# Kernel tuning notes

Hardware: AMD Instinct MI355X
Metric: run time of the kernel (lower is better)

Reference implementation:

```python
import jax, jax.numpy as jnp
import numpy as np

N_NODES = 50000
N_EDGES = 800000
N_FEAT = 128
D_HID = 128
N_CLASS = 40


def gcn_conv(x, W, b, src, dst, n_nodes):
    """PyG GCNConv: h = D^{-1/2} (A + I) D^{-1/2} (x @ W) + b.
    src/dst are int arrays [E]; self-loops handled analytically."""
    h = x @ W  # [N, D]
    ones = jnp.ones(src.shape[0], dtype=h.dtype)
    # degree after adding self-loops: 1 + in-degree (edge weights are 1)
    deg = 1.0 + jax.ops.segment_sum(ones, dst, num_segments=n_nodes)
    dinv = jax.lax.rsqrt(deg)  # [N]
    # messages along edges src -> dst with symmetric normalization
    msg = h[src] * (dinv[src] * dinv[dst])[:, None]  # [E, D]
    agg = jax.ops.segment_sum(msg, dst, num_segments=n_nodes)  # [N, D]
    # self-loop contribution: dinv[i]^2 * h[i]
    agg = agg + h * (dinv * dinv)[:, None]
    return agg + b


def setup_inputs() -> dict:
    key = jax.random.key(0)
    ks = jax.random.split(key, 5)
    x = jax.random.normal(ks[0], (N_NODES, N_FEAT), dtype=jnp.float32)
    edge_index = jax.random.randint(ks[1], (2, N_EDGES), 0, N_NODES, dtype=jnp.int64)
    s_in = 1.0 / np.sqrt(N_FEAT)
    s_h = 1.0 / np.sqrt(D_HID)
    W_in = jax.random.normal(ks[2], (N_FEAT, D_HID), dtype=jnp.float32) * s_in
    W1 = jax.random.normal(ks[3], (D_HID, D_HID), dtype=jnp.float32) * s_h
    W_out = jax.random.normal(ks[4], (D_HID, N_CLASS), dtype=jnp.float32) * s_h
    return {
        "x": x,
        "edge_index": edge_index,
        "W_in": W_in,
        "b_in": jnp.zeros((D_HID,), jnp.float32),
        "W1": W1,
        "b1": jnp.zeros((D_HID,), jnp.float32),
        "W_out": W_out,
        "b_out": jnp.zeros((N_CLASS,), jnp.float32),
    }


def reference(x, edge_index, W_in, b_in, W1, b1, W_out, b_out):
    src, dst = edge_index[0], edge_index[1]
    n = x.shape[0]
    # input GCNConv (no activation on input_fc, matching the torch forward)
    h = gcn_conv(x, W_in, b_in, src, dst, n)
    # hidden layer: dropout is identity at eval; relu after conv; normalize=False
    h = jax.nn.relu(gcn_conv(h, W1, b1, src, dst, n))
    out = h @ W_out + b_out
    return jax.nn.log_softmax(out, axis=1)
```

## Files before the change

kernel.cpp:

```cpp
#include <hip/hip_runtime.h>
#include <math.h>


#define THREADS 256

typedef __attribute__((ext_vector_type(8))) short short8v;
typedef __attribute__((ext_vector_type(4))) float float4v;

__device__ __forceinline__ float b2f(unsigned int lo16) {
    return __uint_as_float(lo16 << 16);
}
__device__ __forceinline__ unsigned short f2b(float f) {
    unsigned int u = __float_as_uint(f);
    u += 0x7FFFu + ((u >> 16) & 1u);
    return (unsigned short)(u >> 16);
}

__global__ __launch_bounds__(256) void f_init(const float* __restrict__ x,
                                              const int* __restrict__ idx,
                                              const float* __restrict__ W0,
                                              const float* __restrict__ W1f,
                                              int* __restrict__ flag,
                                              int* __restrict__ cnt,
                                              uint4* __restrict__ wpk0,
                                              uint4* __restrict__ wpk1,
                                              unsigned short* __restrict__ Xb,
                                              int N) {
    int tid = threadIdx.x, bid = blockIdx.x, nb = gridDim.x;
    if (bid == 0 && tid < 64) {
        unsigned long long b = __ballot(idx[2 * tid + 1] == 0);
        if (tid == 0) *flag = (b == 0xFFFFFFFFFFFFFFFFull) ? 1 : 0;
    }
    for (int i = bid * 256 + tid; i < N; i += nb * 256) cnt[i] = 0;
    if (bid < 2) {
        const float* W = bid ? W1f : W0;
        uint4* wpk = bid ? wpk1 : wpk0;
#pragma unroll
        for (int it = 0; it < 8; ++it) {
            int s = it * 256 + tid;
            int ct = s >> 8, kb = (s >> 6) & 3, l = s & 63;
            int col = ct * 16 + (l & 15);
            int k0 = kb * 32 + ((l >> 4) << 3);
            uint4 u;
            u.x = (unsigned int)f2b(W[(k0 + 0) * 128 + col]) | ((unsigned int)f2b(W[(k0 + 1) * 128 + col]) << 16);
            u.y = (unsigned int)f2b(W[(k0 + 2) * 128 + col]) | ((unsigned int)f2b(W[(k0 + 3) * 128 + col]) << 16);
            u.z = (unsigned int)f2b(W[(k0 + 4) * 128 + col]) | ((unsigned int)f2b(W[(k0 + 5) * 128 + col]) << 16);
            u.w = (unsigned int)f2b(W[(k0 + 6) * 128 + col]) | ((unsigned int)f2b(W[(k0 + 7) * 128 + col]) << 16);
            wpk[s] = u;
        }
    }
    int total = N * 32;
    const float4* x4 = (const float4*)x;
    ushort4* xb4 = (ushort4*)Xb;
    for (int i = bid * 256 + tid; i < total; i += nb * 256) {
        float4 v = x4[i];
        ushort4 o;
        o.x = f2b(v.x); o.y = f2b(v.y); o.z = f2b(v.z); o.w = f2b(v.w);
        xb4[i] = o;
    }
}

__device__ __forceinline__ void gemm_body(const unsigned short* __restrict__ Ab,
                                          const uint4* __restrict__ wpk,
                                          unsigned short* __restrict__ outb,
                                          unsigned short* ol, int base, int N) {
    int tid = threadIdx.x;
    int w = tid >> 6, l = tid & 63;
    int lr = l & 15, lq = l >> 4;
    int arow0 = base + w * 16 + lr;
    int arow1 = base + 64 + w * 16 + lr;
    int ar0 = (arow0 < N) ? arow0 : (N - 1);
    int ar1 = (arow1 < N) ? arow1 : (N - 1);

    float4v acc[2][8];
#pragma unroll
    for (int t = 0; t < 2; ++t)
#pragma unroll
        for (int ct = 0; ct < 8; ++ct) acc[t][ct] = (float4v){0.f, 0.f, 0.f, 0.f};

#pragma unroll
    for (int kb = 0; kb < 4; ++kb) {
        uint4 v0 = *(const uint4*)(Ab + (size_t)ar0 * 128 + kb * 32 + lq * 8);
        uint4 v1 = *(const uint4*)(Ab + (size_t)ar1 * 128 + kb * 32 + lq * 8);
        union { uint4 u; short8v s; } c0, c1; c0.u = v0; c1.u = v1;
        short8v af0 = c0.s, af1 = c1.s;
#pragma unroll
        for (int ct = 0; ct < 8; ++ct) {
            uint4 bv = wpk[(ct * 4 + kb) * 64 + l];
            union { uint4 u; short8v s; } cv; cv.u = bv; short8v bf = cv.s;
            acc[0][ct] = __builtin_amdgcn_mfma_f32_16x16x32_bf16(af0, bf, acc[0][ct], 0, 0, 0);
            acc[1][ct] = __builtin_amdgcn_mfma_f32_16x16x32_bf16(af1, bf, acc[1][ct], 0, 0, 0);
        }
    }
#pragma unroll
    for (int t = 0; t < 2; ++t)
#pragma unroll
        for (int ct = 0; ct < 8; ++ct)
#pragma unroll
            for (int r = 0; r < 4; ++r)
                ol[(t * 64 + w * 16 + lq * 4 + r) * 128 + ct * 16 + lr] = f2b(acc[t][ct][r]);
    __syncthreads();
#pragma unroll
    for (int it = 0; it < 8; ++it) {
        int o = it * 4096 + tid * 16;
        int rr = o >> 8, cb = o & 255;
        int gr = base + rr;
        if (gr < N) {
            uint4 v = *(const uint4*)((const char*)ol + o);
            *(uint4*)((char*)outb + (size_t)gr * 256 + cb) = v;
        }
    }
}

__global__ __launch_bounds__(256) void f_g1fp(const unsigned short* __restrict__ Xb,
                                              const uint4* __restrict__ wpk1,
                                              unsigned short* __restrict__ B0,
                                              const int* __restrict__ idx,
                                              const int* __restrict__ flag,
                                              int* __restrict__ cnt,
                                              unsigned int* __restrict__ rec,
                                              int N, int E, int nbg) {
    __shared__ unsigned short ol[128 * 128];
    if ((int)blockIdx.x < nbg) {
        gemm_body(Xb, wpk1, B0, ol, blockIdx.x * 128, N);
        return;
    }
    int e = (blockIdx.x - nbg) * 256 + threadIdx.x;
    if (e >= E) return;
    int f = *flag;
    int src, dst;
    if (f) { src = idx[2 * e]; dst = idx[2 * (E + e)]; }
    else   { src = idx[e];     dst = idx[E + e]; }
    unsigned int pos = (unsigned int)atomicAdd(&cnt[dst], 1);
    rec[e] = ((unsigned int)src << 16) | (pos & 0xFFFFu);
}

__global__ __launch_bounds__(256) void gemm_mfma(const unsigned short* __restrict__ Ab,
                                                 const uint4* __restrict__ wpk,
                                                 unsigned short* __restrict__ outb,
                                                 int N) {
    __shared__ unsigned short ol[128 * 128];
    gemm_body(Ab, wpk, outb, ol, blockIdx.x * 128, N);
}

__global__ __launch_bounds__(256) void scanA(const int* __restrict__ cnt,
                                             int* __restrict__ bsum, int N) {
    __shared__ int wt[4];
    int tid = threadIdx.x, lane = tid & 63, w = tid >> 6;
    int i = blockIdx.x * 256 + tid;
    int v = (i < N) ? cnt[i] : 0;
    int s = v;
#pragma unroll
    for (int off = 1; off < 64; off <<= 1) {
        int t = __shfl_up(s, off);
        if (lane >= off) s += t;
    }
    if (lane == 63) wt[w] = s;
    __syncthreads();
    if (tid == 0) bsum[blockIdx.x] = wt[0] + wt[1] + wt[2] + wt[3];
}

__global__ __launch_bounds__(256) void scanB(int* __restrict__ bsum,
                                             int* __restrict__ boff,
                                             int* __restrict__ rowstart,
                                             int nb, int N) {
    __shared__ int wt[4];
    __shared__ int wo[5];
    int tid = threadIdx.x, lane = tid & 63, w = tid >> 6;
    int v = (tid < nb) ? bsum[tid] : 0;
    int s = v;
#pragma unroll
    for (int off = 1; off < 64; off <<= 1) {
        int t = __shfl_up(s, off);
        if (lane >= off) s += t;
    }
    if (lane == 63) wt[w] = s;
    __syncthreads();
    if (tid == 0) {
        int run = 0;
#pragma unroll
        for (int k = 0; k < 4; ++k) { wo[k] = run; run += wt[k]; }
        wo[4] = run;
    }
    __syncthreads();
    if (tid < nb) boff[tid] = wo[w] + s - v;
    if (tid == 0) rowstart[N] = wo[4];
}

__global__ __launch_bounds__(256) void scanC(const int* __restrict__ cnt,
                                             const int* __restrict__ boff,
                                             int* __restrict__ rowstart,
                                             float* __restrict__ dinv, int N) {
    __shared__ int wt[4];
    __shared__ int wo[4];
    int tid = threadIdx.x, lane = tid & 63, w = tid >> 6;
    int i = blockIdx.x * 256 + tid;
    int v = (i < N) ? cnt[i] : 0;
    int s = v;
#pragma unroll
    for (int off = 1; off < 64; off <<= 1) {
        int t = __shfl_up(s, off);
        if (lane >= off) s += t;
    }
    if (lane == 63) wt[w] = s;
    __syncthreads();
    if (tid == 0) {
        int run = 0;
#pragma unroll
        for (int k = 0; k < 4; ++k) { wo[k] = run; run += wt[k]; }
    }
    __syncthreads();
    if (i < N) {
        rowstart[i] = boff[blockIdx.x] + wo[w] + (s - v);
        dinv[i] = rsqrtf(1.0f + (float)v);
    }
}

__global__ void fill_place(const int* __restrict__ idx, const int* __restrict__ flag,
                           const unsigned int* __restrict__ rec,
                           const int* __restrict__ rowstart,
                           unsigned short* __restrict__ srcs, int E) {
    int e = blockIdx.x * blockDim.x + threadIdx.x;
    if (e >= E) return;
    int f = *flag;
    int dst = f ? idx[2 * (E + e)] : idx[E + e];
    unsigned int r = rec[e];
    srcs[rowstart[dst] + (int)(r & 0xFFFFu)] = (unsigned short)(r >> 16);
}

__global__ __launch_bounds__(256) void agg_node(const unsigned short* __restrict__ hb,
                                                const int* __restrict__ rowstart,
                                                const unsigned short* __restrict__ srcs,
                                                const float* __restrict__ dinv,
                                                const float* __restrict__ b,
                                                unsigned short* __restrict__ outb,
                                                int N, int do_relu) {
    int w = threadIdx.x >> 6, lane = threadIdx.x & 63;
    int node = blockIdx.x * 4 + w;
    if (node >= N) return;
    int beg = rowstart[node], end = rowstart[node + 1];
    float dn = dinv[node];
    int quarter = lane >> 4, q = lane & 15;
    const uint4* hb8 = (const uint4*)hb;
    float a0 = 0.f, a1 = 0.f, a2 = 0.f, a3 = 0.f;
    float a4 = 0.f, a5 = 0.f, a6 = 0.f, a7 = 0.f;

    for (int j0 = beg; j0 < end; j0 += 64) {
        int myj = j0 + lane;
        int ms = 0; float md = 0.f;
        if (myj < end) { ms = (int)srcs[myj]; md = dinv[ms]; }
        int m = min(64, end - j0);
        for (int k = 0; k < m; k += 8) {
            int i0 = k + quarter;
            int i1 = k + 4 + quarter;
            int s0 = __shfl(ms, i0);
            int s1 = __shfl(ms, i1);
            float c0 = dn * __shfl(md, i0);
            float c1 = dn * __shfl(md, i1);
            uint4 v0 = hb8[(size_t)s0 * 16 + q];
            uint4 v1 = hb8[(size_t)s1 * 16 + q];
            a0 += c0 * b2f(v0.x & 0xFFFFu); a1 += c0 * b2f(v0.x >> 16);
            a2 += c0 * b2f(v0.y & 0xFFFFu); a3 += c0 * b2f(v0.y >> 16);
            a4 += c0 * b2f(v0.z & 0xFFFFu); a5 += c0 * b2f(v0.z >> 16);
            a6 += c0 * b2f(v0.w & 0xFFFFu); a7 += c0 * b2f(v0.w >> 16);
            a0 += c1 * b2f(v1.x & 0xFFFFu); a1 += c1 * b2f(v1.x >> 16);
            a2 += c1 * b2f(v1.y & 0xFFFFu); a3 += c1 * b2f(v1.y >> 16);
            a4 += c1 * b2f(v1.z & 0xFFFFu); a5 += c1 * b2f(v1.z >> 16);
            a6 += c1 * b2f(v1.w & 0xFFFFu); a7 += c1 * b2f(v1.w >> 16);
        }
    }
    a0 += __shfl_xor(a0, 32); a1 += __shfl_xor(a1, 32);
    a2 += __shfl_xor(a2, 32); a3 += __shfl_xor(a3, 32);
    a4 += __shfl_xor(a4, 32); a5 += __shfl_xor(a5, 32);
    a6 += __shfl_xor(a6, 32); a7 += __shfl_xor(a7, 32);
    a0 += __shfl_xor(a0, 16); a1 += __shfl_xor(a1, 16);
    a2 += __shfl_xor(a2, 16); a3 += __shfl_xor(a3, 16);
    a4 += __shfl_xor(a4, 16); a5 += __shfl_xor(a5, 16);
    a6 += __shfl_xor(a6, 16); a7 += __shfl_xor(a7, 16);

    if (quarter == 0) {
        uint4 sv = hb8[(size_t)node * 16 + q];
        float d2 = dn * dn;
        float4 b0 = ((const float4*)b)[2 * q];
        float4 b1 = ((const float4*)b)[2 * q + 1];
        float r0 = a0 + d2 * b2f(sv.x & 0xFFFFu) + b0.x;
        float r1 = a1 + d2 * b2f(sv.x >> 16)     + b0.y;
        float r2 = a2 + d2 * b2f(sv.y & 0xFFFFu) + b0.z;
        float r3 = a3 + d2 * b2f(sv.y >> 16)     + b0.w;
        float r4 = a4 + d2 * b2f(sv.z & 0xFFFFu) + b1.x;
        float r5 = a5 + d2 * b2f(sv.z >> 16)     + b1.y;
        float r6 = a6 + d2 * b2f(sv.w & 0xFFFFu) + b1.z;
        float r7 = a7 + d2 * b2f(sv.w >> 16)     + b1.w;
        if (do_relu) {
            r0 = fmaxf(r0, 0.f); r1 = fmaxf(r1, 0.f);
            r2 = fmaxf(r2, 0.f); r3 = fmaxf(r3, 0.f);
            r4 = fmaxf(r4, 0.f); r5 = fmaxf(r5, 0.f);
            r6 = fmaxf(r6, 0.f); r7 = fmaxf(r7, 0.f);
        }
        uint4 o;
        o.x = (unsigned int)f2b(r0) | ((unsigned int)f2b(r1) << 16);
        o.y = (unsigned int)f2b(r2) | ((unsigned int)f2b(r3) << 16);
        o.z = (unsigned int)f2b(r4) | ((unsigned int)f2b(r5) << 16);
        o.w = (unsigned int)f2b(r6) | ((unsigned int)f2b(r7) << 16);
        ((uint4*)outb)[(size_t)node * 16 + q] = o;
    }
}

__global__ __launch_bounds__(256) void out_gemm(const unsigned short* __restrict__ h2b,
                                                const float* __restrict__ Wout,
                                                const float* __restrict__ bout,
                                                float* __restrict__ out, int N) {
    __shared__ float Xt[128 * 128];
    __shared__ float Wl[128 * 40];
    __shared__ float bl[40];
    int tid = threadIdx.x;
    int row0 = blockIdx.x * 128;

    for (int i = tid; i < 128 * 40; i += 256) Wl[i] = Wout[i];
    if (tid < 40) bl[tid] = bout[tid];

    {
        int r = tid >> 1, kh = tid & 1;
        int gr = row0 + r;
#pragma unroll
        for (int i = 0; i < 16; ++i) {
            int k = kh * 64 + i * 4;
            float f0, f1, f2, f3;
            if (gr < N) {
                uint2 qv = ((const uint2*)h2b)[(size_t)gr * 32 + (k >> 2)];
                f0 = b2f(qv.x & 0xFFFFu); f1 = b2f(qv.x >> 16);
                f2 = b2f(qv.y & 0xFFFFu); f3 = b2f(qv.y >> 16);
            } else {
                f0 = f1 = f2 = f3 = 0.f;
            }
            Xt[(k + 0) * 128 + r] = f0;
            Xt[(k + 1) * 128 + r] = f1;
            Xt[(k + 2) * 128 + r] = f2;
            Xt[(k + 3) * 128 + r] = f3;
        }
    }
    __syncthreads();

    int cg = tid & 7;
    int r4 = tid >> 3;
    float bias[5];
#pragma unroll
    for (int c = 0; c < 5; ++c) bias[c] = bl[5 * cg + c];

    float acc[4][5];
#pragma unroll
    for (int j = 0; j < 4; ++j)
#pragma unroll
        for (int c = 0; c < 5; ++c) acc[j][c] = 0.f;

    const float4* Xt4 = (const float4*)Xt;
#pragma unroll 4
    for (int k = 0; k < 128; ++k) {
        float4 xv = Xt4[k * 32 + r4];
        const float* wr = &Wl[k * 40 + 5 * cg];
        float w0 = wr[0], w1 = wr[1], w2 = wr[2], w3 = wr[3], w4 = wr[4];
        float xs[4] = {xv.x, xv.y, xv.z, xv.w};
#pragma unroll
        for (int j = 0; j < 4; ++j) {
            acc[j][0] += xs[j] * w0;
            acc[j][1] += xs[j] * w1;
            acc[j][2] += xs[j] * w2;
            acc[j][3] += xs[j] * w3;
            acc[j][4] += xs[j] * w4;
        }
    }

#pragma unroll
    for (int j = 0; j < 4; ++j) {
        int r = row0 + r4 * 4 + j;
        if (r >= N) continue;
        float v[5];
        float m = -INFINITY;
#pragma unroll
        for (int c = 0; c < 5; ++c) { v[c] = acc[j][c] + bias[c]; m = fmaxf(m, v[c]); }
        m = fmaxf(m, __shfl_xor(m, 1));
        m = fmaxf(m, __shfl_xor(m, 2));
        m = fmaxf(m, __shfl_xor(m, 4));
        float s = 0.f;
#pragma unroll
        for (int c = 0; c < 5; ++c) s += expf(v[c] - m);
        s += __shfl_xor(s, 1);
        s += __shfl_xor(s, 2);
        s += __shfl_xor(s, 4);
        float ls = logf(s);
#pragma unroll
        for (int c = 0; c < 5; ++c) out[(size_t)r * 40 + 5 * cg + c] = v[c] - m - ls;
    }
}

static inline size_t al256(size_t x) { return (x + 255) & ~(size_t)255; }

extern "C" void kernel_launch(void* const* d_in, const int* in_sizes, int n_in,
                              void* d_out, int out_size, void* d_ws, size_t ws_size,
                              hipStream_t stream) {
    const float* x     = (const float*)d_in[0];
    const int*   idx   = (const int*)d_in[1];
    const float* W_in  = (const float*)d_in[2];
    const float* b_in  = (const float*)d_in[3];
    const float* W1    = (const float*)d_in[4];
    const float* b1    = (const float*)d_in[5];
    const float* W_out = (const float*)d_in[6];
    const float* b_out = (const float*)d_in[7];
    float* out = (float*)d_out;

    int N = in_sizes[0] / 128;
    int E = in_sizes[1] / 2;

    char* ws = (char*)d_ws;
    size_t off = 0;
    int* flag = (int*)(ws + off);              off += 256;
    int* cnt = (int*)(ws + off);               off += al256((size_t)N * 4);
    int* rowstart = (int*)(ws + off);          off += al256((size_t)(N + 1) * 4);
    float* dinv = (float*)(ws + off);          off += al256((size_t)N * 4);
    unsigned short* srcs = (unsigned short*)(ws + off); off += al256((size_t)E * 2);
    unsigned int* rec = (unsigned int*)(ws + off);      off += al256((size_t)E * 4);
    int* bsum = (int*)(ws + off);              off += 2048;
    int* boff = (int*)(ws + off);              off += 2048;
    uint4* wpk1 = (uint4*)(ws + off);          off += 32768;
    uint4* wpk2 = (uint4*)(ws + off);          off += 32768;
    unsigned short* Xb = (unsigned short*)(ws + off);   off += (size_t)N * 128 * 2;
    unsigned short* B0 = (unsigned short*)(ws + off);   off += (size_t)N * 128 * 2;
    unsigned short* B1 = (unsigned short*)(ws + off);

    int nb_e = (E + THREADS - 1) / THREADS;
    int nb_n = (N + THREADS - 1) / THREADS;
    int nb_g = (N + 127) / 128;
    int nb_a = (N + 3) / 4;

    f_init<<<256, THREADS, 0, stream>>>(x, idx, W_in, W1, flag, cnt, wpk1, wpk2, Xb, N);
    f_g1fp<<<nb_g + nb_e, THREADS, 0, stream>>>(Xb, wpk1, B0, idx, flag, cnt, rec,
                                                N, E, nb_g);
    scanA<<<nb_n, THREADS, 0, stream>>>(cnt, bsum, N);
    scanB<<<1, THREADS, 0, stream>>>(bsum, boff, rowstart, nb_n, N);
    scanC<<<nb_n, THREADS, 0, stream>>>(cnt, boff, rowstart, dinv, N);
    fill_place<<<nb_e, THREADS, 0, stream>>>(idx, flag, rec, rowstart, srcs, E);

    agg_node<<<nb_a, THREADS, 0, stream>>>(B0, rowstart, srcs, dinv, b_in, B1, N, 0);
    gemm_mfma<<<nb_g, THREADS, 0, stream>>>(B1, wpk2, B0, N);
    agg_node<<<nb_a, THREADS, 0, stream>>>(B0, rowstart, srcs, dinv, b1, B1, N, 1);
    out_gemm<<<nb_g, THREADS, 0, stream>>>(B1, W_out, b_out, out, N);
}
```

Before: 256.0 us.

## Make GEMM per-wave with private LDS, and fold the scan offset pass into scanC

```diff
diff --git a/kernel.cpp b/kernel.cpp
--- a/kernel.cpp
+++ b/kernel.cpp
@@ -60,53 +60,44 @@
     }
 }
 
-__device__ __forceinline__ void gemm_body(const unsigned short* __restrict__ Ab,
+__device__ __forceinline__ void gemm_wave(const unsigned short* __restrict__ Ab,
                                           const uint4* __restrict__ wpk,
                                           unsigned short* __restrict__ outb,
-                                          unsigned short* ol, int base, int N) {
-    int tid = threadIdx.x;
-    int w = tid >> 6, l = tid & 63;
+                                          unsigned short* olw,
+                                          int row0, int N) {
+    int l = threadIdx.x & 63;
     int lr = l & 15, lq = l >> 4;
-    int arow0 = base + w * 16 + lr;
-    int arow1 = base + 64 + w * 16 + lr;
-    int ar0 = (arow0 < N) ? arow0 : (N - 1);
-    int ar1 = (arow1 < N) ? arow1 : (N - 1);
-
-    float4v acc[2][8];
-#pragma unroll
-    for (int t = 0; t < 2; ++t)
-#pragma unroll
-        for (int ct = 0; ct < 8; ++ct) acc[t][ct] = (float4v){0.f, 0.f, 0.f, 0.f};
+    int arow = row0 + lr;
+    int ar = (arow < N) ? arow : (N - 1);
+
+    float4v acc[8];
+#pragma unroll
+    for (int ct = 0; ct < 8; ++ct) acc[ct] = (float4v){0.f, 0.f, 0.f, 0.f};
 
 #pragma unroll
     for (int kb = 0; kb < 4; ++kb) {
-        uint4 v0 = *(const uint4*)(Ab + (size_t)ar0 * 128 + kb * 32 + lq * 8);
-        uint4 v1 = *(const uint4*)(Ab + (size_t)ar1 * 128 + kb * 32 + lq * 8);
-        union { uint4 u; short8v s; } c0, c1; c0.u = v0; c1.u = v1;
-        short8v af0 = c0.s, af1 = c1.s;
+        uint4 v = *(const uint4*)(Ab + (size_t)ar * 128 + kb * 32 + lq * 8);
+        union { uint4 u; short8v s; } cv; cv.u = v;
+        short8v af = cv.s;
 #pragma unroll
         for (int ct = 0; ct < 8; ++ct) {
             uint4 bv = wpk[(ct * 4 + kb) * 64 + l];
-            union { uint4 u; short8v s; } cv; cv.u = bv; short8v bf = cv.s;
-            acc[0][ct] = __builtin_amdgcn_mfma_f32_16x16x32_bf16(af0, bf, acc[0][ct], 0, 0, 0);
-            acc[1][ct] = __builtin_amdgcn_mfma_f32_16x16x32_bf16(af1, bf, acc[1][ct], 0, 0, 0);
-        }
-    }
-#pragma unroll
-    for (int t = 0; t < 2; ++t)
-#pragma unroll
-        for (int ct = 0; ct < 8; ++ct)
-#pragma unroll
-            for (int r = 0; r < 4; ++r)
-                ol[(t * 64 + w * 16 + lq * 4 + r) * 128 + ct * 16 + lr] = f2b(acc[t][ct][r]);
-    __syncthreads();
-#pragma unroll
-    for (int it = 0; it < 8; ++it) {
-        int o = it * 4096 + tid * 16;
+            union { uint4 u; short8v s; } cb; cb.u = bv;
+            acc[ct] = __builtin_amdgcn_mfma_f32_16x16x32_bf16(af, cb.s, acc[ct], 0, 0, 0);
+        }
+    }
+#pragma unroll
+    for (int ct = 0; ct < 8; ++ct)
+#pragma unroll
+        for (int r = 0; r < 4; ++r)
+            olw[(lq * 4 + r) * 128 + ct * 16 + lr] = f2b(acc[ct][r]);
+#pragma unroll
+    for (int it = 0; it < 4; ++it) {
+        int o = it * 1024 + l * 16;
         int rr = o >> 8, cb = o & 255;
-        int gr = base + rr;
+        int gr = row0 + rr;
         if (gr < N) {
-            uint4 v = *(const uint4*)((const char*)ol + o);
+            uint4 v = *(const uint4*)((const char*)olw + o);
             *(uint4*)((char*)outb + (size_t)gr * 256 + cb) = v;
         }
     }
@@ -120,9 +111,10 @@
                                               int* __restrict__ cnt,
                                               unsigned int* __restrict__ rec,
                                               int N, int E, int nbg) {
-    __shared__ unsigned short ol[128 * 128];
+    __shared__ unsigned short ol[4][16 * 128];
     if ((int)blockIdx.x < nbg) {
-        gemm_body(Xb, wpk1, B0, ol, blockIdx.x * 128, N);
+        int w = threadIdx.x >> 6;
+        gemm_wave(Xb, wpk1, B0, ol[w], blockIdx.x * 64 + w * 16, N);
         return;
     }
     int e = (blockIdx.x - nbg) * 256 + threadIdx.x;
@@ -139,8 +131,9 @@
                                                  const uint4* __restrict__ wpk,
                                                  unsigned short* __restrict__ outb,
                                                  int N) {
-    __shared__ unsigned short ol[128 * 128];
-    gemm_body(Ab, wpk, outb, ol, blockIdx.x * 128, N);
+    __shared__ unsigned short ol[4][16 * 128];
+    int w = threadIdx.x >> 6;
+    gemm_wave(Ab, wpk, outb, ol[w], blockIdx.x * 64 + w * 16, N);
 }
 
 __global__ __launch_bounds__(256) void scanA(const int* __restrict__ cnt,
@@ -160,14 +153,24 @@
     if (tid == 0) bsum[blockIdx.x] = wt[0] + wt[1] + wt[2] + wt[3];
 }
 
-__global__ __launch_bounds__(256) void scanB(int* __restrict__ bsum,
-                                             int* __restrict__ boff,
-                                             int* __restrict__ rowstart,
-                                             int nb, int N) {
+__global__ __launch_bounds__(256) void scanC2(const int* __restrict__ cnt,
+                                              const int* __restrict__ bsum,
+                                              int* __restrict__ rowstart,
+                                              float* __restrict__ dinv,
+                                              int N, int nb, int E) {
     __shared__ int wt[4];
-    __shared__ int wo[5];
+    __shared__ int wo[4];
+    __shared__ int blkoff;
     int tid = threadIdx.x, lane = tid & 63, w = tid >> 6;
-    int v = (tid < nb) ? bsum[tid] : 0;
+    if (tid < 64) {
+        int acc = 0;
+        for (int j = lane; j < (int)blockIdx.x; j += 64) acc += bsum[j];
+#pragma unroll
+        for (int off = 32; off > 0; off >>= 1) acc += __shfl_xor(acc, off);
+        if (lane == 0) blkoff = acc;
+    }
+    int i = blockIdx.x * 256 + tid;
+    int v = (i < N) ? cnt[i] : 0;
     int s = v;
 #pragma unroll
     for (int off = 1; off < 64; off <<= 1) {
@@ -180,40 +183,13 @@
         int run = 0;
 #pragma unroll
         for (int k = 0; k < 4; ++k) { wo[k] = run; run += wt[k]; }
-        wo[4] = run;
-    }
-    __syncthreads();
-    if (tid < nb) boff[tid] = wo[w] + s - v;
-    if (tid == 0) rowstart[N] = wo[4];
-}
-
-__global__ __launch_bounds__(256) void scanC(const int* __restrict__ cnt,
-                                             const int* __restrict__ boff,
-                                             int* __restrict__ rowstart,
-                                             float* __restrict__ dinv, int N) {
-    __shared__ int wt[4];
-    __shared__ int wo[4];
-    int tid = threadIdx.x, lane = tid & 63, w = tid >> 6;
-    int i = blockIdx.x * 256 + tid;
-    int v = (i < N) ? cnt[i] : 0;
-    int s = v;
-#pragma unroll
-    for (int off = 1; off < 64; off <<= 1) {
-        int t = __shfl_up(s, off);
-        if (lane >= off) s += t;
-    }
-    if (lane == 63) wt[w] = s;
-    __syncthreads();
-    if (tid == 0) {
-        int run = 0;
-#pragma unroll
-        for (int k = 0; k < 4; ++k) { wo[k] = run; run += wt[k]; }
     }
     __syncthreads();
     if (i < N) {
-        rowstart[i] = boff[blockIdx.x] + wo[w] + (s - v);
+        rowstart[i] = blkoff + wo[w] + (s - v);
         dinv[i] = rsqrtf(1.0f + (float)v);
     }
+    if (blockIdx.x == 0 && tid == 0) rowstart[N] = E;
 }
 
 __global__ void fill_place(const int* __restrict__ idx, const int* __restrict__ flag,
@@ -420,7 +396,6 @@
     unsigned short* srcs = (unsigned short*)(ws + off); off += al256((size_t)E * 2);
     unsigned int* rec = (unsigned int*)(ws + off);      off += al256((size_t)E * 4);
     int* bsum = (int*)(ws + off);              off += 2048;
-    int* boff = (int*)(ws + off);              off += 2048;
     uint4* wpk1 = (uint4*)(ws + off);          off += 32768;
     uint4* wpk2 = (uint4*)(ws + off);          off += 32768;
     unsigned short* Xb = (unsigned short*)(ws + off);   off += (size_t)N * 128 * 2;
@@ -429,19 +404,19 @@
 
     int nb_e = (E + THREADS - 1) / THREADS;
     int nb_n = (N + THREADS - 1) / THREADS;
-    int nb_g = (N + 127) / 128;
+    int nb_g = (N + 63) / 64;
     int nb_a = (N + 3) / 4;
+    int nb_o = (N + 127) / 128;
 
     f_init<<<256, THREADS, 0, stream>>>(x, idx, W_in, W1, flag, cnt, wpk1, wpk2, Xb, N);
     f_g1fp<<<nb_g + nb_e, THREADS, 0, stream>>>(Xb, wpk1, B0, idx, flag, cnt, rec,
                                                 N, E, nb_g);
     scanA<<<nb_n, THREADS, 0, stream>>>(cnt, bsum, N);
-    scanB<<<1, THREADS, 0, stream>>>(bsum, boff, rowstart, nb_n, N);
-    scanC<<<nb_n, THREADS, 0, stream>>>(cnt, boff, rowstart, dinv, N);
+    scanC2<<<nb_n, THREADS, 0, stream>>>(cnt, bsum, rowstart, dinv, N, nb_n, E);
     fill_place<<<nb_e, THREADS, 0, stream>>>(idx, flag, rec, rowstart, srcs, E);
 
     agg_node<<<nb_a, THREADS, 0, stream>>>(B0, rowstart, srcs, dinv, b_in, B1, N, 0);
     gemm_mfma<<<nb_g, THREADS, 0, stream>>>(B1, wpk2, B0, N);
     agg_node<<<nb_a, THREADS, 0, stream>>>(B0, rowstart, srcs, dinv, b1, B1, N, 1);
-    out_gemm<<<nb_g, THREADS, 0, stream>>>(B1, W_out, b_out, out, N);
-}
+    out_gemm<<<nb_o, THREADS, 0, stream>>>(B1, W_out, b_out, out, N);
+}
```

Measured after the change: 254.6 us. About the same (-0.5%).
